# Kernel optimization log

Hardware: AMD Instinct MI355X
Metric: run time of the kernel (lower is better)

## Reference

```python
import jax, jax.numpy as jnp
import numpy as np

LN_EPS = 1e-4
NEG = -1e10


def setup_inputs() -> dict:
    key = jax.random.key(0)
    ks = jax.random.split(key, 5)
    b, p, d, i, h, m = 2, 2048, 1024, 16, 64, 4096
    sd = 1.0 / np.sqrt(d)
    return {
        "x": jax.random.normal(ks[0], (b, p, d), jnp.float32),
        "W_K": jax.random.normal(ks[1], (i, h, d), jnp.float32) * sd,
        "W_Q": jax.random.normal(ks[2], (i, h, d), jnp.float32) * sd,
        "W_V": jax.random.normal(ks[3], (i, h, d), jnp.float32) * sd,
        "w_ln": jnp.ones((d,), jnp.float32),
        "b_ln": jnp.zeros((d,), jnp.float32),
        "W_in": jax.random.normal(ks[4], (m, d), jnp.float32) * sd,
        "b_in": jnp.zeros((m,), jnp.float32),
        "W_out": jax.random.normal(jax.random.fold_in(key, 9), (d, m), jnp.float32) * sd,
        "b_out": jnp.zeros((d,), jnp.float32),
    }


def reference(x, W_K, W_Q, W_V, w_ln, b_ln, W_in, b_in, W_out, b_out):
    b, p, d = x.shape
    # --- attention (unscaled softmax, scaled=False in TransformerBlock) ---
    k = jnp.einsum('ihd,bpd->biph', W_K, x)
    q = jnp.einsum('ihd,bpd->biph', W_Q, x)
    v = jnp.einsum('ihd,bpd->biph', W_V, x)
    scores = jnp.einsum('biph,biqh->biqp', k, q)  # [b,i,q_pos,k_pos]
    causal = jnp.tril(jnp.ones((p, p), bool))      # k_pos <= q_pos
    masked = jnp.where(causal, scores, NEG)
    attn = jax.nn.softmax(masked, axis=-1)
    z = jnp.einsum('biph,biqp->biqh', v, attn)     # [b,i,q,h]
    z_flat = jnp.transpose(z, (0, 2, 1, 3)).reshape(b, p, d)  # b q (i h)
    x = x + z_flat
    # --- custom LayerNorm: unbiased std, eps added to std ---
    c = x - jnp.mean(x, axis=-1, keepdims=True)
    std = jnp.sqrt(jnp.sum(c * c, axis=-1, keepdims=True) / (d - 1))
    x = c / (std + LN_EPS) * w_ln + b_ln
    # --- MLP with residual ---
    hpre = jnp.einsum('md,bpd->bpm', W_in, x) + b_in
    hact = jax.nn.gelu(hpre, approximate=False)
    mlp = jnp.einsum('dm,bpm->bpd', W_out, hact) + b_out
    return x + mlp
```

## Files before the change

### kernel.cpp

```cpp
#include <hip/hip_runtime.h>
#include <hip/hip_bf16.h>

typedef __bf16 bf16x8 __attribute__((ext_vector_type(8)));
typedef float f32x4 __attribute__((ext_vector_type(4)));

#define BAR() __builtin_amdgcn_s_barrier()
#define MEMFENCE() asm volatile("" ::: "memory")
#define VMCNT8() asm volatile("s_waitcnt vmcnt(8)" ::: "memory")
#define VMCNT2() asm volatile("s_waitcnt vmcnt(2)" ::: "memory")
#define VMCNT0() asm volatile("s_waitcnt vmcnt(0)" ::: "memory")

__device__ __forceinline__ void gload_lds16(const void* g, void* l) {
  __builtin_amdgcn_global_load_lds(
      (const __attribute__((address_space(1))) void*)g,
      (__attribute__((address_space(3))) void*)l, 16, 0, 0);
}

__global__ __launch_bounds__(256) void k_f2b_all(
    const float* __restrict__ x, const float* __restrict__ wk,
    const float* __restrict__ wq, const float* __restrict__ wv,
    const float* __restrict__ wi, const float* __restrict__ wo,
    __bf16* __restrict__ xb, __bf16* __restrict__ wqkv,
    __bf16* __restrict__ winb, __bf16* __restrict__ woutb) {
  int i = (blockIdx.x * 256 + threadIdx.x) * 4;
  const float* s; __bf16* d; int off;
  if (i < 4194304)       { s = x;  d = xb;             off = i; }
  else if (i < 5242880)  { s = wk; d = wqkv;           off = i - 4194304; }
  else if (i < 6291456)  { s = wq; d = wqkv + 1048576; off = i - 5242880; }
  else if (i < 7340032)  { s = wv; d = wqkv + 2097152; off = i - 6291456; }
  else if (i < 11534336) { s = wi; d = winb;           off = i - 7340032; }
  else                   { s = wo; d = woutb;          off = i - 11534336; }
  const float4 v = *(const float4*)(s + off);
  d[off + 0] = (__bf16)v.x;
  d[off + 1] = (__bf16)v.y;
  d[off + 2] = (__bf16)v.z;
  d[off + 3] = (__bf16)v.w;
}

template <int EPI, int WM, int WN, int MI, int NI>
__global__ __launch_bounds__(WM * WN * 64, 2) void k_gemm(
    const __bf16* __restrict__ A, const __bf16* __restrict__ B, int N, int K,
    int NT, const float* __restrict__ bias, const float* __restrict__ resid,
    float* __restrict__ outf, __bf16* __restrict__ outb,
    __bf16* __restrict__ ok, __bf16* __restrict__ oq, __bf16* __restrict__ ovt) {
  constexpr int BM = WM * MI * 16, BN = WN * NI * 16;
  constexpr int LA = BM / (8 * WM * WN);
  constexpr int LB = BN / (8 * WM * WN);
  __shared__ __align__(16) __bf16 lds[2][(BM + BN) * 64];
  const int tid = threadIdx.x;
  const int lane = tid & 63, wid = tid >> 6;
  const int wr = wid / WN, wc = wid % WN;
  const int lr = lane & 15, lh = lane >> 4;
  const int bid = blockIdx.x;
  const int cpx = gridDim.x >> 3;
  const int sid = (bid & 7) * cpx + (bid >> 3);
  const int mt = sid / NT, nt = sid - mt * NT;
  const int m0 = mt * BM, n0 = nt * BN;
  const int nkt = K >> 6;

  auto stage = [&](int t, int bufi) {
    const int k0 = t << 6;
    __bf16* As = lds[bufi];
    __bf16* Bs = lds[bufi] + BM * 64;
#pragma unroll
    for (int j = 0; j < LA; ++j) {
      int chunk = (wid * LA + j) * 64 + lane;
      int row = chunk >> 3, c8 = chunk & 7;
      int g8 = c8 ^ (row & 7);
      gload_lds16(A + (size_t)(m0 + row) * K + k0 + g8 * 8, As + chunk * 8);
    }
#pragma unroll
    for (int j = 0; j < LB; ++j) {
      int chunk = (wid * LB + j) * 64 + lane;
      int row = chunk >> 3, c8 = chunk & 7;
      int g8 = c8 ^ (row & 7);
      gload_lds16(B + (size_t)(n0 + row) * K + k0 + g8 * 8, Bs + chunk * 8);
    }
  };

  f32x4 acc[MI][NI] = {};
  stage(0, 0);
  stage(1, 1);
  VMCNT8();
  BAR();

  for (int t = 0; t < nkt; ++t) {
    const __bf16* As = lds[t & 1];
    const __bf16* Bs = lds[t & 1] + BM * 64;
#pragma unroll
    for (int ks = 0; ks < 2; ++ks) {
      bf16x8 af[MI], bf[NI];
#pragma unroll
      for (int mi = 0; mi < MI; ++mi) {
        int row = wr * (MI * 16) + mi * 16 + lr;
        af[mi] = *(const bf16x8*)&As[row * 64 + (((ks * 4 + lh) ^ (row & 7)) * 8)];
      }
#pragma unroll
      for (int ni = 0; ni < NI; ++ni) {
        int row = wc * (NI * 16) + ni * 16 + lr;
        bf[ni] = *(const bf16x8*)&Bs[row * 64 + (((ks * 4 + lh) ^ (row & 7)) * 8)];
      }
#pragma unroll
      for (int mi = 0; mi < MI; ++mi)
#pragma unroll
        for (int ni = 0; ni < NI; ++ni)
          acc[mi][ni] = __builtin_amdgcn_mfma_f32_16x16x32_bf16(
              af[mi], bf[ni], acc[mi][ni], 0, 0, 0);
    }
    MEMFENCE();
    BAR();
    if (t + 2 < nkt) {
      stage(t + 2, t & 1);
      VMCNT8();
    } else {
      VMCNT0();
    }
    BAR();
  }

#pragma unroll
  for (int mi = 0; mi < MI; ++mi) {
#pragma unroll
    for (int j = 0; j < 4; ++j) {
      const int row = m0 + wr * (MI * 16) + mi * 16 + lh * 4 + j;
#pragma unroll
      for (int ni = 0; ni < NI; ++ni) {
        const int col = n0 + wc * (NI * 16) + ni * 16 + lr;
        float v = acc[mi][ni][j];
        if constexpr (EPI == 0) {
          const int which = col >> 10, c = col & 1023;
          const int ih = c >> 6, hh = c & 63;
          const int bb = row >> 11, pp = row & 2047;
          const int bi = bb * 16 + ih;
          if (which == 0)
            ok[((size_t)bi * 2048 + pp) * 64 + hh] = (__bf16)v;
          else if (which == 1)
            oq[((size_t)bi * 2048 + pp) * 64 + hh] = (__bf16)v;
          else
            ovt[((size_t)bi * 64 + hh) * 2048 + pp] = (__bf16)v;
        } else if constexpr (EPI == 1) {
          float h = v + bias[col];
          float g = 0.5f * h * (1.f + erff(h * 0.70710678118f));
          outb[(size_t)row * N + col] = (__bf16)g;
        } else {
          outf[(size_t)row * N + col] = v + bias[col] + resid[(size_t)row * N + col];
        }
      }
    }
  }
}

__global__ __launch_bounds__(512) void k_attn(const __bf16* __restrict__ kb,
                                              const __bf16* __restrict__ qb,
                                              const __bf16* __restrict__ vt,
                                              float* __restrict__ z) {
  const int tid = threadIdx.x;
  const int lane = tid & 63, w = tid >> 6;
  const int lr = lane & 15, lh = lane >> 4;
  const int wgid = blockIdx.x;
  const int xcd = wgid & 7;
  const int t = wgid >> 3;
  const int bi = xcd + 8 * (t & 3);
  const int qblk = t >> 2;
  const int b = bi >> 4, ih = bi & 15;
  const int q0B = qblk * 256;
  const int qw = q0B + w * 32;
  const __bf16* kbase = kb + (size_t)bi * 2048 * 64;
  const __bf16* qbase = qb + (size_t)bi * 2048 * 64;
  const __bf16* vbase = vt + (size_t)bi * 64 * 2048;

  __shared__ __align__(16) __bf16 kv[2][2][64 * 64];
  __shared__ __align__(16) __bf16 plds[8][2][16 * 76];

  const int nk = (q0B >> 6) + 4;

  auto stage = [&](int kt, int bufi) {
    const int k0 = kt << 6;
    const int row = tid >> 3, c8 = tid & 7;
    const int g8 = c8 ^ (row & 7);
    gload_lds16(kbase + (size_t)(k0 + row) * 64 + g8 * 8,
                &kv[bufi][0][tid * 8]);
    gload_lds16(vbase + (size_t)row * 2048 + k0 + g8 * 8,
                &kv[bufi][1][tid * 8]);
  };

  bf16x8 aq[2][2];
#pragma unroll
  for (int tl = 0; tl < 2; ++tl)
#pragma unroll
    for (int ks = 0; ks < 2; ++ks)
      aq[tl][ks] = *(const bf16x8*)(qbase + (size_t)(qw + tl * 16 + lr) * 64 + ks * 32 + lh * 8);

  f32x4 o[2][4] = {};
  float lsum[2][4] = {};

  stage(0, 0);
  stage(1, 1);
  VMCNT2();
  BAR();

  for (int kt = 0; kt < nk; ++kt) {
    const int k0 = kt << 6;
    const __bf16* Ks = kv[kt & 1][0];
    const __bf16* Vs = kv[kt & 1][1];
    const bool act = (k0 <= qw + 31);

    if (act) {
      bf16x8 bk[4][2];
#pragma unroll
      for (int n = 0; n < 4; ++n) {
        int r = n * 16 + lr;
#pragma unroll
        for (int ks = 0; ks < 2; ++ks)
          bk[n][ks] = *(const bf16x8*)&Ks[r * 64 + (((ks * 4 + lh) ^ (r & 7)) * 8)];
      }
      f32x4 s[2][4] = {};
#pragma unroll
      for (int ks = 0; ks < 2; ++ks)
#pragma unroll
        for (int n = 0; n < 4; ++n) {
          s[0][n] = __builtin_amdgcn_mfma_f32_16x16x32_bf16(aq[0][ks], bk[n][ks], s[0][n], 0, 0, 0);
          s[1][n] = __builtin_amdgcn_mfma_f32_16x16x32_bf16(aq[1][ks], bk[n][ks], s[1][n], 0, 0, 0);
        }

      bf16x8 bv[4][2];
#pragma unroll
      for (int ht = 0; ht < 4; ++ht) {
        int r = ht * 16 + lr;
#pragma unroll
        for (int ks = 0; ks < 2; ++ks)
          bv[ht][ks] = *(const bf16x8*)&Vs[r * 64 + (((ks * 4 + lh) ^ (r & 7)) * 8)];
      }

      if (k0 + 63 > qw) {
#pragma unroll
        for (int tl = 0; tl < 2; ++tl)
#pragma unroll
          for (int n = 0; n < 4; ++n)
#pragma unroll
            for (int j = 0; j < 4; ++j) {
              int qpos = qw + tl * 16 + lh * 4 + j;
              int kpos = k0 + n * 16 + lr;
              if (kpos > qpos) s[tl][n][j] = -1e10f;
            }
      }

#pragma unroll
      for (int tl = 0; tl < 2; ++tl) {
#pragma unroll
        for (int n = 0; n < 4; ++n)
#pragma unroll
          for (int j = 0; j < 4; ++j) s[tl][n][j] = __expf(s[tl][n][j]);
#pragma unroll
        for (int j = 0; j < 4; ++j)
          lsum[tl][j] += (s[tl][0][j] + s[tl][1][j]) + (s[tl][2][j] + s[tl][3][j]);
      }

#pragma unroll
      for (int tl = 0; tl < 2; ++tl)
#pragma unroll
        for (int n = 0; n < 4; ++n)
#pragma unroll
          for (int j = 0; j < 4; ++j)
            plds[w][tl][(lh * 4 + j) * 76 + n * 16 + lr] = (__bf16)s[tl][n][j];
      bf16x8 pa[2][2];
#pragma unroll
      for (int tl = 0; tl < 2; ++tl)
#pragma unroll
        for (int ks = 0; ks < 2; ++ks)
          pa[tl][ks] = *(const bf16x8*)&plds[w][tl][lr * 76 + ks * 32 + lh * 8];
#pragma unroll
      for (int ks = 0; ks < 2; ++ks)
#pragma unroll
        for (int ht = 0; ht < 4; ++ht) {
          o[0][ht] = __builtin_amdgcn_mfma_f32_16x16x32_bf16(pa[0][ks], bv[ht][ks], o[0][ht], 0, 0, 0);
          o[1][ht] = __builtin_amdgcn_mfma_f32_16x16x32_bf16(pa[1][ks], bv[ht][ks], o[1][ht], 0, 0, 0);
        }
    }

    MEMFENCE();
    BAR();
    if (kt + 2 < nk) {
      stage(kt + 2, kt & 1);
      VMCNT2();
    } else {
      VMCNT0();
    }
    BAR();
  }

#pragma unroll
  for (int m = 1; m < 16; m <<= 1)
#pragma unroll
    for (int tl = 0; tl < 2; ++tl)
#pragma unroll
      for (int j = 0; j < 4; ++j) lsum[tl][j] += __shfl_xor(lsum[tl][j], m);

  float* zr = z + (size_t)b * 2048 * 1024;
#pragma unroll
  for (int tl = 0; tl < 2; ++tl)
#pragma unroll
    for (int j = 0; j < 4; ++j) {
      float inv = 1.f / lsum[tl][j];
      int q = qw + tl * 16 + lh * 4 + j;
#pragma unroll
      for (int ht = 0; ht < 4; ++ht)
        zr[(size_t)q * 1024 + ih * 64 + ht * 16 + lr] = o[tl][ht][j] * inv;
    }
}

__global__ __launch_bounds__(256) void k_ln(const float* __restrict__ x,
                                            const float* __restrict__ z,
                                            const float* __restrict__ wln,
                                            const float* __restrict__ bln,
                                            float* __restrict__ y,
                                            __bf16* __restrict__ yb) {
  const int row = blockIdx.x;
  const int t = threadIdx.x;
  const int lane = t & 63, wid = t >> 6;
  const float4 xv = ((const float4*)(x + (size_t)row * 1024))[t];
  const float4 zv = ((const float4*)(z + (size_t)row * 1024))[t];
  float v0 = xv.x + zv.x, v1 = xv.y + zv.y, v2 = xv.z + zv.z, v3 = xv.w + zv.w;
  __shared__ float red[4];
  float s = v0 + v1 + v2 + v3;
#pragma unroll
  for (int m = 1; m < 64; m <<= 1) s += __shfl_xor(s, m);
  if (lane == 0) red[wid] = s;
  __syncthreads();
  const float mean = (red[0] + red[1] + red[2] + red[3]) * (1.f / 1024.f);
  const float c0 = v0 - mean, c1 = v1 - mean, c2 = v2 - mean, c3 = v3 - mean;
  float ss = c0 * c0 + c1 * c1 + c2 * c2 + c3 * c3;
#pragma unroll
  for (int m = 1; m < 64; m <<= 1) ss += __shfl_xor(ss, m);
  __syncthreads();
  if (lane == 0) red[wid] = ss;
  __syncthreads();
  const float var = (red[0] + red[1] + red[2] + red[3]) * (1.f / 1023.f);
  const float inv = 1.f / (sqrtf(var) + 1e-4f);
  const float4 wv = ((const float4*)wln)[t];
  const float4 bv = ((const float4*)bln)[t];
  float y0 = c0 * inv * wv.x + bv.x;
  float y1 = c1 * inv * wv.y + bv.y;
  float y2 = c2 * inv * wv.z + bv.z;
  float y3 = c3 * inv * wv.w + bv.w;
  float4 yo; yo.x = y0; yo.y = y1; yo.z = y2; yo.w = y3;
  ((float4*)(y + (size_t)row * 1024))[t] = yo;
  __bf16* yd = yb + (size_t)row * 1024 + t * 4;
  yd[0] = (__bf16)y0; yd[1] = (__bf16)y1; yd[2] = (__bf16)y2; yd[3] = (__bf16)y3;
}

extern "C" void kernel_launch(void* const* d_in, const int* in_sizes, int n_in,
                              void* d_out, int out_size, void* d_ws, size_t ws_size,
                              hipStream_t stream) {
  const float* x = (const float*)d_in[0];
  const float* W_K = (const float*)d_in[1];
  const float* W_Q = (const float*)d_in[2];
  const float* W_V = (const float*)d_in[3];
  const float* w_ln = (const float*)d_in[4];
  const float* b_ln = (const float*)d_in[5];
  const float* W_in = (const float*)d_in[6];
  const float* b_in = (const float*)d_in[7];
  const float* W_out = (const float*)d_in[8];
  const float* b_out = (const float*)d_in[9];
  float* out = (float*)d_out;

  char* ws = (char*)d_ws;
  const size_t NEEDED = 132120576;
  if (ws_size < NEEDED) return;

  __bf16* xb   = (__bf16*)(ws);
  __bf16* wqkv = (__bf16*)(ws + 8388608);
  __bf16* winb = (__bf16*)(ws + 14680064);
  __bf16* woutb= (__bf16*)(ws + 23068672);
  __bf16* kbuf = (__bf16*)(ws + 31457280);
  __bf16* qbuf = (__bf16*)(ws + 39845888);
  __bf16* vtb  = (__bf16*)(ws + 48234496);
  float*  zb   = (float*)(ws + 56623104);
  float*  yf   = (float*)(ws + 73400320);
  __bf16* ybb  = (__bf16*)(ws + 90177536);
  __bf16* hact = (__bf16*)(ws + 98566144);

  k_f2b_all<<<15360, 256, 0, stream>>>(x, W_K, W_Q, W_V, W_in, W_out,
                                       xb, wqkv, winb, woutb);

  k_gemm<0, 2, 4, 8, 4><<<192, 512, 0, stream>>>(xb, wqkv, 3072, 1024, 12,
                                                 nullptr, nullptr, nullptr,
                                                 nullptr, kbuf, qbuf, vtb);
  k_attn<<<dim3(256), 512, 0, stream>>>(kbuf, qbuf, vtb, zb);
  k_ln<<<4096, 256, 0, stream>>>(x, zb, w_ln, b_ln, yf, ybb);
  k_gemm<1, 2, 4, 8, 4><<<256, 512, 0, stream>>>(ybb, winb, 4096, 1024, 16,
                                                 b_in, nullptr, nullptr, hact,
                                                 nullptr, nullptr, nullptr);
  k_gemm<2, 2, 2, 4, 4><<<256, 256, 0, stream>>>(hact, woutb, 1024, 4096, 8,
                                                 b_out, yf, out, nullptr,
                                                 nullptr, nullptr, nullptr);
}
```

Measured before the change: 235.9 us.

## Add 8-wave 256x256 GEMM with half-tile staged ping-pong pipeline for QKV and MLP-in

Adds a new GEMM kernel, k_g8, that computes 256x256 tiles with 8 waves. It splits each 64-wide K tile into halves and interleaves LDS fragment reads, asynchronous global-to-LDS loads of the next halves, and MFMA bursts under raised wave priority, with barriers between phases. The QKV projection and the MLP up-projection with GELU now use it, while the down-projection keeps the old kernel. The aim is to overlap memory traffic with matrix-core work at finer granularity. The cost is more barriers per K step and heavier register use for the 8x4 accumulator tile.

```diff
diff --git a/kernel.cpp b/kernel.cpp
--- a/kernel.cpp
+++ b/kernel.cpp
@@ -7,6 +7,7 @@
 #define BAR() __builtin_amdgcn_s_barrier()
 #define MEMFENCE() asm volatile("" ::: "memory")
 #define VMCNT8() asm volatile("s_waitcnt vmcnt(8)" ::: "memory")
+#define VMCNT4() asm volatile("s_waitcnt vmcnt(4)" ::: "memory")
 #define VMCNT2() asm volatile("s_waitcnt vmcnt(2)" ::: "memory")
 #define VMCNT0() asm volatile("s_waitcnt vmcnt(0)" ::: "memory")
 
@@ -35,6 +36,153 @@
   d[off + 1] = (__bf16)v.y;
   d[off + 2] = (__bf16)v.z;
   d[off + 3] = (__bf16)v.w;
+}
+
+template <int EPI>
+__global__ __launch_bounds__(512) void k_g8(
+    const __bf16* __restrict__ A, const __bf16* __restrict__ B, int N, int K,
+    int NT, const float* __restrict__ bias,
+    float* __restrict__ outf, __bf16* __restrict__ outb,
+    __bf16* __restrict__ ok, __bf16* __restrict__ oq, __bf16* __restrict__ ovt) {
+  __shared__ __align__(16) __bf16 lds8[2][32768];
+  const int tid = threadIdx.x;
+  const int lane = tid & 63, wid = tid >> 6;
+  const int wm = wid >> 2, wn = wid & 3;
+  const int lr = lane & 15, lh = lane >> 4;
+  const int bid = blockIdx.x;
+  const int cpx = gridDim.x >> 3;
+  const int sid = (bid & 7) * cpx + (bid >> 3);
+  const int mt = sid / NT, nt = sid - mt * NT;
+  const int m0 = mt * 256, n0 = nt * 256;
+  const int nkt = K >> 6;
+
+  auto stageH = [&](int mat, int h, int t) {
+    const int k0 = t << 6;
+    const __bf16* G = mat ? B : A;
+    const int g0 = mat ? n0 : m0;
+    __bf16* L = &lds8[t & 1][mat * 16384 + h * 8192];
+#pragma unroll
+    for (int jj = 0; jj < 2; ++jj) {
+      int local = (wid * 2 + jj) * 64 + lane;
+      int r = local >> 2;
+      int cc = (local & 3) ^ ((r & 3) ^ ((r >> 2) & 3));
+      gload_lds16(G + (size_t)(g0 + r) * K + k0 + (h * 4 + cc) * 8,
+                  L + local * 8);
+    }
+  };
+
+  f32x4 acc[8][4] = {};
+
+  stageH(0, 0, 0); stageH(1, 0, 0); stageH(0, 1, 0); stageH(1, 1, 0);
+  stageH(0, 0, 1); stageH(1, 0, 1);
+  VMCNT4();
+  MEMFENCE(); BAR();
+
+  for (int t = 0; t < nkt; ++t) {
+    const __bf16* La = lds8[t & 1];
+    const __bf16* Lb = lds8[t & 1] + 16384;
+    bf16x8 a0[4], a1[4], bb[4];
+#pragma unroll
+    for (int i = 0; i < 4; ++i) {
+      int r = wm * 128 + i * 16 + lr;
+      a0[i] = *(const bf16x8*)&La[r * 32 + ((lh ^ ((r & 3) ^ ((r >> 2) & 3))) * 8)];
+    }
+#pragma unroll
+    for (int j = 0; j < 4; ++j) {
+      int r = wn * 64 + j * 16 + lr;
+      bb[j] = *(const bf16x8*)&Lb[r * 32 + ((lh ^ ((r & 3) ^ ((r >> 2) & 3))) * 8)];
+    }
+    if (t + 1 < nkt) stageH(0, 1, t + 1);
+    MEMFENCE(); BAR();
+    __builtin_amdgcn_s_setprio(1);
+#pragma unroll
+    for (int i = 0; i < 4; ++i)
+#pragma unroll
+      for (int j = 0; j < 4; ++j)
+        acc[i][j] = __builtin_amdgcn_mfma_f32_16x16x32_bf16(a0[i], bb[j], acc[i][j], 0, 0, 0);
+    __builtin_amdgcn_s_setprio(0);
+    MEMFENCE(); BAR();
+#pragma unroll
+    for (int i = 0; i < 4; ++i) {
+      int r = wm * 128 + (4 + i) * 16 + lr;
+      a1[i] = *(const bf16x8*)&La[r * 32 + ((lh ^ ((r & 3) ^ ((r >> 2) & 3))) * 8)];
+    }
+    if (t + 1 < nkt) stageH(1, 1, t + 1);
+    MEMFENCE(); BAR();
+    __builtin_amdgcn_s_setprio(1);
+#pragma unroll
+    for (int i = 0; i < 4; ++i)
+#pragma unroll
+      for (int j = 0; j < 4; ++j)
+        acc[4 + i][j] = __builtin_amdgcn_mfma_f32_16x16x32_bf16(a1[i], bb[j], acc[4 + i][j], 0, 0, 0);
+    __builtin_amdgcn_s_setprio(0);
+    MEMFENCE(); BAR();
+#pragma unroll
+    for (int i = 0; i < 4; ++i) {
+      int r = wm * 128 + i * 16 + lr;
+      a0[i] = *(const bf16x8*)&La[8192 + r * 32 + ((lh ^ ((r & 3) ^ ((r >> 2) & 3))) * 8)];
+    }
+#pragma unroll
+    for (int j = 0; j < 4; ++j) {
+      int r = wn * 64 + j * 16 + lr;
+      bb[j] = *(const bf16x8*)&Lb[8192 + r * 32 + ((lh ^ ((r & 3) ^ ((r >> 2) & 3))) * 8)];
+    }
+    if (t + 2 < nkt) stageH(0, 0, t + 2);
+    MEMFENCE(); BAR();
+    __builtin_amdgcn_s_setprio(1);
+#pragma unroll
+    for (int i = 0; i < 4; ++i)
+#pragma unroll
+      for (int j = 0; j < 4; ++j)
+        acc[i][j] = __builtin_amdgcn_mfma_f32_16x16x32_bf16(a0[i], bb[j], acc[i][j], 0, 0, 0);
+    __builtin_amdgcn_s_setprio(0);
+    MEMFENCE(); BAR();
+#pragma unroll
+    for (int i = 0; i < 4; ++i) {
+      int r = wm * 128 + (4 + i) * 16 + lr;
+      a1[i] = *(const bf16x8*)&La[8192 + r * 32 + ((lh ^ ((r & 3) ^ ((r >> 2) & 3))) * 8)];
+    }
+    if (t + 2 < nkt) stageH(1, 0, t + 2);
+    MEMFENCE(); BAR();
+    __builtin_amdgcn_s_setprio(1);
+#pragma unroll
+    for (int i = 0; i < 4; ++i)
+#pragma unroll
+      for (int j = 0; j < 4; ++j)
+        acc[4 + i][j] = __builtin_amdgcn_mfma_f32_16x16x32_bf16(a1[i], bb[j], acc[4 + i][j], 0, 0, 0);
+    __builtin_amdgcn_s_setprio(0);
+    if (t + 2 < nkt) { VMCNT4(); } else { VMCNT0(); }
+    MEMFENCE(); BAR();
+  }
+
+#pragma unroll
+  for (int mi = 0; mi < 8; ++mi) {
+#pragma unroll
+    for (int jj = 0; jj < 4; ++jj) {
+      const int row = m0 + wm * 128 + mi * 16 + lh * 4 + jj;
+#pragma unroll
+      for (int ni = 0; ni < 4; ++ni) {
+        const int col = n0 + wn * 64 + ni * 16 + lr;
+        float v = acc[mi][ni][jj];
+        if constexpr (EPI == 0) {
+          const int which = col >> 10, c = col & 1023;
+          const int ih = c >> 6, hh = c & 63;
+          const int bb2 = row >> 11, pp = row & 2047;
+          const int bi = bb2 * 16 + ih;
+          if (which == 0)
+            ok[((size_t)bi * 2048 + pp) * 64 + hh] = (__bf16)v;
+          else if (which == 1)
+            oq[((size_t)bi * 2048 + pp) * 64 + hh] = (__bf16)v;
+          else
+            ovt[((size_t)bi * 64 + hh) * 2048 + pp] = (__bf16)v;
+        } else {
+          float h = v + bias[col];
+          float g = 0.5f * h * (1.f + erff(h * 0.70710678118f));
+          outb[(size_t)row * N + col] = (__bf16)g;
+        }
+      }
+    }
+  }
 }
 
 template <int EPI, int WM, int WN, int MI, int NI>
@@ -127,23 +275,12 @@
       for (int ni = 0; ni < NI; ++ni) {
         const int col = n0 + wc * (NI * 16) + ni * 16 + lr;
         float v = acc[mi][ni][j];
-        if constexpr (EPI == 0) {
-          const int which = col >> 10, c = col & 1023;
-          const int ih = c >> 6, hh = c & 63;
-          const int bb = row >> 11, pp = row & 2047;
-          const int bi = bb * 16 + ih;
-          if (which == 0)
-            ok[((size_t)bi * 2048 + pp) * 64 + hh] = (__bf16)v;
-          else if (which == 1)
-            oq[((size_t)bi * 2048 + pp) * 64 + hh] = (__bf16)v;
-          else
-            ovt[((size_t)bi * 64 + hh) * 2048 + pp] = (__bf16)v;
+        if constexpr (EPI == 2) {
+          outf[(size_t)row * N + col] = v + bias[col] + resid[(size_t)row * N + col];
         } else if constexpr (EPI == 1) {
           float h = v + bias[col];
           float g = 0.5f * h * (1.f + erff(h * 0.70710678118f));
           outb[(size_t)row * N + col] = (__bf16)g;
-        } else {
-          outf[(size_t)row * N + col] = v + bias[col] + resid[(size_t)row * N + col];
         }
       }
     }
@@ -383,14 +520,12 @@
   k_f2b_all<<<15360, 256, 0, stream>>>(x, W_K, W_Q, W_V, W_in, W_out,
                                        xb, wqkv, winb, woutb);
 
-  k_gemm<0, 2, 4, 8, 4><<<192, 512, 0, stream>>>(xb, wqkv, 3072, 1024, 12,
-                                                 nullptr, nullptr, nullptr,
-                                                 nullptr, kbuf, qbuf, vtb);
+  k_g8<0><<<192, 512, 0, stream>>>(xb, wqkv, 3072, 1024, 12, nullptr,
+                                   nullptr, nullptr, kbuf, qbuf, vtb);
   k_attn<<<dim3(256), 512, 0, stream>>>(kbuf, qbuf, vtb, zb);
   k_ln<<<4096, 256, 0, stream>>>(x, zb, w_ln, b_ln, yf, ybb);
-  k_gemm<1, 2, 4, 8, 4><<<256, 512, 0, stream>>>(ybb, winb, 4096, 1024, 16,
-                                                 b_in, nullptr, nullptr, hact,
-                                                 nullptr, nullptr, nullptr);
+  k_g8<1><<<256, 512, 0, stream>>>(ybb, winb, 4096, 1024, 16, b_in,
+                                   nullptr, hact, nullptr, nullptr, nullptr);
   k_gemm<2, 2, 2, 4, 4><<<256, 256, 0, stream>>>(hact, woutb, 1024, 4096, 8,
                                                  b_out, yf, out, nullptr,
                                                  nullptr, nullptr, nullptr);
```

Result: slower. 243.8 us (+3.4%).
